# Kernel tuning notes

Measured on AMD Instinct MI355X. Metric: run time of the kernel, lower is better.

Reference implementation:

```python
import jax, jax.numpy as jnp
import numpy as np

N_FRAG = 1_000_000
CELL_N = 1000
GENE_N = 500
N_GENES = 5000
H = 100   # hidden dims
E = 100   # embedding dims


def setup_inputs() -> dict:
    key = jax.random.key(0)
    ks = jax.random.split(key, 16)
    coords = jax.random.randint(ks[0], (N_FRAG, 2), 0, 1000, dtype=jnp.int64 if jax.config.jax_enable_x64 else jnp.int32)
    cxg_ix = jnp.sort(jax.random.randint(ks[1], (N_FRAG,), 0, CELL_N * GENE_N))
    gene_ix = jax.random.randint(ks[2], (GENE_N,), 0, N_GENES)
    stdv_in = 1.0 / np.sqrt(2)
    stdv_h = 1.0 / np.sqrt(H)
    u = lambda k, shape, s: jax.random.uniform(k, shape, jnp.float32, -s, s)
    W0 = u(ks[3], (2, H), stdv_in); b0 = u(ks[4], (H,), stdv_in)
    W1 = u(ks[5], (H, H), stdv_h); b1 = u(ks[6], (H,), stdv_h)
    W2 = u(ks[7], (H, H), stdv_h); b2 = u(ks[8], (H,), stdv_h)
    W3 = u(ks[9], (H, E), stdv_h); b3 = u(ks[10], (E,), stdv_h)
    weight1 = u(ks[11], (N_GENES, E), stdv_h / 100.0)  # torch init: stdv/100
    bias1 = jax.random.normal(ks[12], (N_GENES,), jnp.float32)  # mean gene expression
    return {
        "fragment_coordinates": coords,
        "fragment_cellxgene_ix": cxg_ix,
        "cell_n": CELL_N,
        "gene_n": GENE_N,
        "gene_ix": gene_ix,
        "W0": W0, "b0": b0, "W1": W1, "b1": b1,
        "W2": W2, "b2": b2, "W3": W3, "b3": b3,
        "weight1": weight1, "bias1": bias1,
    }


def reference(fragment_coordinates, fragment_cellxgene_ix, cell_n, gene_n, gene_ix,
              W0, b0, W1, b1, W2, b2, W3, b3, weight1, bias1):
    # FragmentEmbedder: 4-layer MLP on scaled coordinates
    x = fragment_coordinates.astype(jnp.float32) / 1000.0          # [F, 2]
    h = jax.nn.relu(x @ W0 + b0)
    h = jax.nn.relu(h @ W1 + b1)
    h = jax.nn.relu(h @ W2 + b2)
    emb = h @ W3 + b3                                              # [F, E]
    # EmbeddingGenePooler: segment-sum into cell x gene bins
    pooled = jax.ops.segment_sum(emb, fragment_cellxgene_ix,
                                 num_segments=cell_n * gene_n)     # [C*G, E]
    cg = pooled.reshape(cell_n, gene_n, -1)                        # [C, G, E]
    # EmbeddingToExpression: gene-specific weighted sum + bias
    out = jnp.einsum('cge,ge->cg', cg, weight1[gene_ix]) + bias1[gene_ix]
    return out
```

## Files before the change

kernel.cpp:

```cpp
#include <hip/hip_runtime.h>
#include <hip/hip_bf16.h>

typedef __attribute__((ext_vector_type(4))) short s16x4;
typedef __attribute__((ext_vector_type(4))) float f32x4;
typedef __attribute__((ext_vector_type(8))) unsigned short u16x8;
typedef __attribute__((ext_vector_type(8))) __bf16 bf16x8;

#define GENE_N     500
#define WG_STRIDE  112
#define WG_OFF_BYTES 81920
#define OFF_B_BYTES 3584
#define OFF_C_BYTES 68096
#define NFRAG_TOTAL 91
#define LDS_BYTES   64512

__device__ __forceinline__ unsigned short f2bf(float x){
  __hip_bfloat16 h = __float2bfloat16(x);
  return *reinterpret_cast<unsigned short*>(&h);
}

__device__ __forceinline__ f32x4 mfma16(s16x4 a, s16x4 b, f32x4 c){
  return __builtin_amdgcn_mfma_f32_16x16x16bf16_1k(a, b, c, 0, 0, 0);
}
__device__ __forceinline__ f32x4 mfma32(bf16x8 a, bf16x8 b, f32x4 c){
  return __builtin_amdgcn_mfma_f32_16x16x32_bf16(a, b, c, 0, 0, 0);
}

__global__ void init_out(const int* __restrict__ gene_ix,
                         const float* __restrict__ bias1,
                         float* __restrict__ out, int n){
  int t = blockIdx.x*blockDim.x + threadIdx.x;
  if (t < n) out[t] = bias1[gene_ix[t % GENE_N]];
}

__global__ void prep_weights(const float* __restrict__ W0, const float* __restrict__ b0,
                             const float* __restrict__ W1, const float* __restrict__ b1,
                             const float* __restrict__ W2, const float* __restrict__ b2,
                             const float* __restrict__ W3, const float* __restrict__ b3,
                             unsigned short* __restrict__ wsW){
  int t = blockIdx.x*blockDim.x + threadIdx.x;
  if (t >= NFRAG_TOTAL*64) return;
  int fr = t >> 6, lane = t & 63;
  int grp = lane >> 4, row = lane & 15;

  if (fr < 7){
    int up = fr*16 + row;
    unsigned short* dst = wsW + (fr*64 + lane)*4;
    #pragma unroll
    for (int i = 0; i < 4; ++i){
      int k = grp*4 + i;
      float val = 0.f;
      if (up < 100){
        if (k < 2)       val = W0[k*100 + up];
        else if (k == 2) val = b0[up];
      }
      dst[i] = f2bf(val);
    }
  } else if (fr < 70){
    int fb = fr - 7;
    int L = fb/21, m = (fb%21)/3, q = fb%3;
    const float* W = (L==0)?W1:(L==1)?W2:W3;
    int up = m*16 + row;
    unsigned short* dst = wsW + OFF_B_BYTES/2 + (fb*64 + lane)*8;
    #pragma unroll
    for (int i = 0; i < 8; ++i){
      int k = 32*q + ((i < 4) ? (grp*4 + i) : (16 + grp*4 + (i-4)));
      float val = 0.f;
      if (up < 100 && k < 100) val = W[k*100 + up];
      dst[i] = f2bf(val);
    }
  } else {
    int fc = fr - 70;
    int L = fc/7, m = fc%7;
    const float* W = (L==0)?W1:(L==1)?W2:W3;
    const float* B = (L==0)?b1:(L==1)?b2:b3;
    int up = m*16 + row;
    unsigned short* dst = wsW + OFF_C_BYTES/2 + (fc*64 + lane)*4;
    #pragma unroll
    for (int i = 0; i < 4; ++i){
      int k = 96 + grp*4 + i;
      float val = 0.f;
      if (up < 100){
        if (k < 100)       val = W[k*100 + up];
        else if (k == 100) val = B[up];
      }
      dst[i] = f2bf(val);
    }
  }
}

__global__ void prep_wg(const int* __restrict__ gene_ix,
                        const float* __restrict__ weight1,
                        float* __restrict__ wg){
  int t = blockIdx.x*blockDim.x + threadIdx.x;
  if (t >= GENE_N*WG_STRIDE) return;
  int g = t / WG_STRIDE, e = t % WG_STRIDE;
  wg[t] = (e < 100) ? weight1[gene_ix[g]*100 + e] : 0.f;
}


__device__ __forceinline__ unsigned fbits(float x){ return __builtin_bit_cast(unsigned, x); }

__device__ __forceinline__ void pack_relu2(const f32x4* __restrict__ acc,
                                           unsigned* __restrict__ pl,
                                           unsigned* __restrict__ ph, bool selb){
  #pragma unroll
  for (int m = 0; m < 7; ++m){
    unsigned u0 = fbits(fmaxf(acc[m][0], 0.f)) + 0x8000u;
    unsigned u1 = fbits(fmaxf(acc[m][1], 0.f)) + 0x8000u;
    unsigned u2 = fbits(fmaxf(acc[m][2], 0.f)) + 0x8000u;
    unsigned u3 = fbits(fmaxf(acc[m][3], 0.f)) + 0x8000u;
    unsigned lo = __builtin_amdgcn_perm(u1, u0, 0x07060302u);
    unsigned hi = __builtin_amdgcn_perm(u3, u2, 0x07060302u);
    if (m == 6) lo = selb ? ((lo & 0xFFFF0000u) | 0x3F80u) : lo;
    pl[m] = lo; ph[m] = hi;
  }
}

__device__ __forceinline__ bf16x8 catB(unsigned a0, unsigned a1, unsigned b0, unsigned b1){
  uint4 u; u.x = a0; u.y = a1; u.z = b0; u.w = b1;
  return __builtin_bit_cast(bf16x8, u);
}

__device__ __forceinline__ bf16x8 ldsFrag(const unsigned char* lds, int fb, int lane){
  return *(const bf16x8*)(lds + fb*1024 + lane*16);
}

template<int L>
__device__ __forceinline__ void hidden1(const unsigned char* __restrict__ lds,
                                        const unsigned short* __restrict__ tails,
                                        int lane,
                                        const unsigned* __restrict__ pl,
                                        const unsigned* __restrict__ ph,
                                        f32x4* __restrict__ acc){
  const f32x4 zero = {0.f,0.f,0.f,0.f};
  uint2 tl[7];
  #pragma unroll
  for (int m = 0; m < 7; ++m)
    tl[m] = *(const uint2*)(tails + ((L*7 + m)*64 + lane)*4);

  bf16x8 B0 = catB(pl[0], ph[0], pl[1], ph[1]);
  bf16x8 B1 = catB(pl[2], ph[2], pl[3], ph[3]);
  bf16x8 B2 = catB(pl[4], ph[4], pl[5], ph[5]);
  uint2 t6; t6.x = pl[6]; t6.y = ph[6];
  s16x4 b6 = __builtin_bit_cast(s16x4, t6);

  #pragma unroll
  for (int m = 0; m < 7; ++m){
    const int fb = L*21 + m*3;
    bf16x8 w0 = ldsFrag(lds, fb,   lane);
    bf16x8 w1 = ldsFrag(lds, fb+1, lane);
    bf16x8 w2 = ldsFrag(lds, fb+2, lane);
    f32x4 a = mfma32(w0, B0, zero);
    a = mfma32(w1, B1, a);
    a = mfma32(w2, B2, a);
    acc[m] = a;
  }
  #pragma unroll
  for (int m = 0; m < 7; ++m)
    acc[m] = mfma16(__builtin_bit_cast(s16x4, tl[m]), b6, acc[m]);
}

__device__ __forceinline__ void epi_store(const f32x4* __restrict__ acc,
                                          const float* __restrict__ wg,
                                          int grp, int lane, int f, int nfrag,
                                          int cxgv, float* __restrict__ out){
  int gbin = cxgv % GENE_N;
  const float* wrow = wg + gbin*WG_STRIDE + grp*4;
  float s = 0.f;
  #pragma unroll
  for (int m = 0; m < 7; ++m){
    float4 w = *(const float4*)(wrow + m*16);
    s += acc[m][0]*w.x + acc[m][1]*w.y + acc[m][2]*w.z + acc[m][3]*w.w;
  }
  s += __shfl_xor(s, 16);
  s += __shfl_xor(s, 32);
  if (lane < 16 && f < nfrag) atomicAdd(out + cxgv, s);
}

__device__ __forceinline__ s16x4 build_bx(int2 cd){
  s16x4 v;
  v[0] = (short)f2bf((float)cd.x * 1e-3f);
  v[1] = (short)f2bf((float)cd.y * 1e-3f);
  v[2] = (short)0x3F80;
  v[3] = 0;
  return v;
}

__global__ __launch_bounds__(256, 1)
void frag_mlp_pool(const int* __restrict__ coords, const int* __restrict__ cxg,
                   const unsigned short* __restrict__ wsW,
                   const float* __restrict__ wg,
                   float* __restrict__ out, int nfrag, int ntiles){
  __shared__ __align__(16) unsigned char ldsW[LDS_BYTES];

  {
    const uint4* src = (const uint4*)((const unsigned char*)wsW + OFF_B_BYTES);
    uint4* dst = (uint4*)ldsW;
    for (int t = threadIdx.x; t < LDS_BYTES/16; t += 256) dst[t] = src[t];
  }
  __syncthreads();

  const int lane = threadIdx.x & 63;
  const int wid  = threadIdx.x >> 6;
  const int grp = lane >> 4, row = lane & 15;
  const bool selb = (grp == 1);

  const s16x4* wfA = (const s16x4*)wsW;
  const unsigned short* tails = wsW + OFF_C_BYTES/2;

  s16x4 A0[7];
  #pragma unroll
  for (int i = 0; i < 7; ++i) A0[i] = wfA[i*64 + lane];

  const f32x4 zero = {0.f,0.f,0.f,0.f};
  const int lastf = nfrag - 1;
  const int gw = blockIdx.x*4 + wid;
  const int nw = gridDim.x*4;

  int f0 = gw*16 + row;
  int c0 = (f0 < nfrag) ? f0 : lastf;
  int2 cdN = ((const int2*)coords)[c0];
  int  xgN = cxg[c0];

  for (int t = gw; t < ntiles; t += nw){
    int f = t*16 + row;
    int2 cd = cdN;
    int  xg = xgN;

    int tn = t + nw;
    int fn = tn*16 + row;
    int cn = (fn < nfrag) ? fn : lastf;
    cdN = ((const int2*)coords)[cn];
    xgN = cxg[cn];

    s16x4 bx = build_bx(cd);
    f32x4 acc[7];
    #pragma unroll
    for (int m = 0; m < 7; ++m) acc[m] = mfma16(A0[m], bx, zero);

    unsigned pl[7], ph[7];
    pack_relu2(acc, pl, ph, selb);
    hidden1<0>(ldsW, tails, lane, pl, ph, acc);
    pack_relu2(acc, pl, ph, selb);
    hidden1<1>(ldsW, tails, lane, pl, ph, acc);
    pack_relu2(acc, pl, ph, selb);
    hidden1<2>(ldsW, tails, lane, pl, ph, acc);

    epi_store(acc, wg, grp, lane, f, nfrag, xg, out);
  }
}

extern "C" void kernel_launch(void* const* d_in, const int* in_sizes, int n_in,
                              void* d_out, int out_size, void* d_ws, size_t ws_size,
                              hipStream_t stream){
  const int* coords  = (const int*)d_in[0];
  const int* cxg     = (const int*)d_in[1];
  const int* gene_ix = (const int*)d_in[4];
  const float* W0 = (const float*)d_in[5];
  const float* b0 = (const float*)d_in[6];
  const float* W1 = (const float*)d_in[7];
  const float* b1 = (const float*)d_in[8];
  const float* W2 = (const float*)d_in[9];
  const float* b2 = (const float*)d_in[10];
  const float* W3 = (const float*)d_in[11];
  const float* b3 = (const float*)d_in[12];
  const float* weight1 = (const float*)d_in[13];
  const float* bias1   = (const float*)d_in[14];

  int nfrag  = in_sizes[1];
  int ntiles = (nfrag + 15) / 16;

  unsigned short* wsW = (unsigned short*)d_ws;
  float* wg = (float*)((char*)d_ws + WG_OFF_BYTES);
  float* out = (float*)d_out;

  hipLaunchKernelGGL(init_out, dim3((out_size + 255)/256), dim3(256), 0, stream,
                     gene_ix, bias1, out, out_size);
  hipLaunchKernelGGL(prep_weights, dim3((NFRAG_TOTAL*64 + 255)/256), dim3(256), 0, stream,
                     W0, b0, W1, b1, W2, b2, W3, b3, wsW);
  hipLaunchKernelGGL(prep_wg, dim3((GENE_N*WG_STRIDE + 255)/256), dim3(256), 0, stream,
                     gene_ix, weight1, wg);
  hipLaunchKernelGGL(frag_mlp_pool, dim3(512), dim3(256), 0, stream,
                     coords, cxg, wsW, wg, out, nfrag, ntiles);
}
```

Baseline: 204.9 us.

## Move bias tails into LDS and stream third-layer weights from global

The LDS weight region now holds only the first two hidden layers' main fragments plus the bias/tail fragments for all layers, instead of all three layers' fragments. The tails no longer come from global memory inside each layer. The third hidden layer's main weights are read from global (L2-cached) with a three-slot rotating register prefetch interleaved with the MFMAs. The aim is to cut per-tile global tail loads and shrink the LDS footprint. The cost is more VGPR pressure and global-load latency in the last layer.

```diff
diff --git a/kernel.cpp b/kernel.cpp
--- a/kernel.cpp
+++ b/kernel.cpp
@@ -12,7 +12,9 @@
 #define OFF_B_BYTES 3584
 #define OFF_C_BYTES 68096
 #define NFRAG_TOTAL 91
-#define LDS_BYTES   64512
+#define LDS_W12    43008
+#define LDS_TAILS  10752
+#define LDS_BYTES  (LDS_W12 + LDS_TAILS)
 
 __device__ __forceinline__ unsigned short f2bf(float x){
   __hip_bfloat16 h = __float2bfloat16(x);
@@ -127,18 +129,12 @@
 }
 
 template<int L>
-__device__ __forceinline__ void hidden1(const unsigned char* __restrict__ lds,
-                                        const unsigned short* __restrict__ tails,
-                                        int lane,
-                                        const unsigned* __restrict__ pl,
-                                        const unsigned* __restrict__ ph,
-                                        f32x4* __restrict__ acc){
+__device__ __forceinline__ void hidden01(const unsigned char* __restrict__ lds,
+                                         int lane,
+                                         const unsigned* __restrict__ pl,
+                                         const unsigned* __restrict__ ph,
+                                         f32x4* __restrict__ acc){
   const f32x4 zero = {0.f,0.f,0.f,0.f};
-  uint2 tl[7];
-  #pragma unroll
-  for (int m = 0; m < 7; ++m)
-    tl[m] = *(const uint2*)(tails + ((L*7 + m)*64 + lane)*4);
-
   bf16x8 B0 = catB(pl[0], ph[0], pl[1], ph[1]);
   bf16x8 B1 = catB(pl[2], ph[2], pl[3], ph[3]);
   bf16x8 B2 = catB(pl[4], ph[4], pl[5], ph[5]);
@@ -157,8 +153,49 @@
     acc[m] = a;
   }
   #pragma unroll
-  for (int m = 0; m < 7; ++m)
-    acc[m] = mfma16(__builtin_bit_cast(s16x4, tl[m]), b6, acc[m]);
+  for (int m = 0; m < 7; ++m){
+    uint2 tl = *(const uint2*)(lds + LDS_W12 + ((L*7 + m)*64 + lane)*8);
+    acc[m] = mfma16(__builtin_bit_cast(s16x4, tl), b6, acc[m]);
+  }
+}
+
+__device__ __forceinline__ void hidden2(const unsigned char* __restrict__ lds,
+                                        const u16x8* __restrict__ w3, int lane,
+                                        const unsigned* __restrict__ pl,
+                                        const unsigned* __restrict__ ph,
+                                        f32x4* __restrict__ acc){
+  const f32x4 zero = {0.f,0.f,0.f,0.f};
+  bf16x8 B0 = catB(pl[0], ph[0], pl[1], ph[1]);
+  bf16x8 B1 = catB(pl[2], ph[2], pl[3], ph[3]);
+  bf16x8 B2 = catB(pl[4], ph[4], pl[5], ph[5]);
+  uint2 t6; t6.x = pl[6]; t6.y = ph[6];
+  s16x4 b6 = __builtin_bit_cast(s16x4, t6);
+
+  u16x8 w[3][3];
+  #pragma unroll
+  for (int j = 0; j < 3; ++j) w[0][j] = w3[(0 + j)*64 + lane];
+  #pragma unroll
+  for (int j = 0; j < 3; ++j) w[1][j] = w3[(3 + j)*64 + lane];
+  #pragma unroll
+  for (int j = 0; j < 3; ++j) w[2][j] = w3[(6 + j)*64 + lane];
+
+  #pragma unroll
+  for (int m = 0; m < 7; ++m){
+    const int s = m % 3;
+    f32x4 a = mfma32(__builtin_bit_cast(bf16x8, w[s][0]), B0, zero);
+    a = mfma32(__builtin_bit_cast(bf16x8, w[s][1]), B1, a);
+    a = mfma32(__builtin_bit_cast(bf16x8, w[s][2]), B2, a);
+    acc[m] = a;
+    if (m + 3 < 7){
+      #pragma unroll
+      for (int j = 0; j < 3; ++j) w[s][j] = w3[((m+3)*3 + j)*64 + lane];
+    }
+  }
+  #pragma unroll
+  for (int m = 0; m < 7; ++m){
+    uint2 tl = *(const uint2*)(lds + LDS_W12 + ((2*7 + m)*64 + lane)*8);
+    acc[m] = mfma16(__builtin_bit_cast(s16x4, tl), b6, acc[m]);
+  }
 }
 
 __device__ __forceinline__ void epi_store(const f32x4* __restrict__ acc,
@@ -195,9 +232,12 @@
   __shared__ __align__(16) unsigned char ldsW[LDS_BYTES];
 
   {
-    const uint4* src = (const uint4*)((const unsigned char*)wsW + OFF_B_BYTES);
-    uint4* dst = (uint4*)ldsW;
-    for (int t = threadIdx.x; t < LDS_BYTES/16; t += 256) dst[t] = src[t];
+    const uint4* src1 = (const uint4*)((const unsigned char*)wsW + OFF_B_BYTES);
+    uint4* dst1 = (uint4*)ldsW;
+    for (int t = threadIdx.x; t < LDS_W12/16; t += 256) dst1[t] = src1[t];
+    const uint4* src2 = (const uint4*)((const unsigned char*)wsW + OFF_C_BYTES);
+    uint4* dst2 = (uint4*)(ldsW + LDS_W12);
+    for (int t = threadIdx.x; t < LDS_TAILS/16; t += 256) dst2[t] = src2[t];
   }
   __syncthreads();
 
@@ -207,7 +247,7 @@
   const bool selb = (grp == 1);
 
   const s16x4* wfA = (const s16x4*)wsW;
-  const unsigned short* tails = wsW + OFF_C_BYTES/2;
+  const u16x8* w3  = (const u16x8*)(wsW + OFF_B_BYTES/2) + 42*64;
 
   s16x4 A0[7];
   #pragma unroll
@@ -241,11 +281,11 @@
 
     unsigned pl[7], ph[7];
     pack_relu2(acc, pl, ph, selb);
-    hidden1<0>(ldsW, tails, lane, pl, ph, acc);
+    hidden01<0>(ldsW, lane, pl, ph, acc);
     pack_relu2(acc, pl, ph, selb);
-    hidden1<1>(ldsW, tails, lane, pl, ph, acc);
+    hidden01<1>(ldsW, lane, pl, ph, acc);
     pack_relu2(acc, pl, ph, selb);
-    hidden1<2>(ldsW, tails, lane, pl, ph, acc);
+    hidden2(ldsW, w3, lane, pl, ph, acc);
 
     epi_store(acc, wg, grp, lane, f, nfrag, xg, out);
   }
```

After: 195.7 us. -4.5%, faster.
